# Kernel tuning notes

Hardware: AMD Instinct MI355X
Metric: run time of the kernel (lower is better)

## Reference

```python
import jax, jax.numpy as jnp
import numpy as np
import math

B, N, D, H, E, EDGE_DIM, GEO_DIM = 32, 256, 512, 8, 1024, 256, 64
HD = D // H

def _lin(x, W, b):
    return x @ W.T + b

def _ln(x, g, b):
    m = x.mean(-1, keepdims=True)
    v = ((x - m) ** 2).mean(-1, keepdims=True)
    return (x - m) * jax.lax.rsqrt(v + 1e-5) * g + b

def setup_inputs() -> dict:
    key = jax.random.key(0)
    ks = jax.random.split(key, 20)
    p = lambda k, s: jax.random.normal(k, s, jnp.float32) * 0.02
    inp = {
        'x': jax.random.normal(ks[0], (B, N, D), jnp.float32),
        'node_masks': jnp.ones((B, N), jnp.float32),
        'relation_edges': jax.random.randint(ks[1], (B, E, 2), 0, N),
        'relation_masks': (jax.random.uniform(ks[2], (B, E)) > 0.2).astype(jnp.float32),
        'relation_embeddings': jax.random.normal(ks[3], (B, E, EDGE_DIM), jnp.float32),
        'relation_geo_features': jax.random.normal(ks[4], (B, E, GEO_DIM), jnp.float32),
        'Wq': p(ks[5], (D, D)), 'bq': jnp.zeros((D,), jnp.float32),
        'Wk': p(ks[6], (D, D)), 'bk': jnp.zeros((D,), jnp.float32),
        'Wv': p(ks[7], (D, D)), 'bv': jnp.zeros((D,), jnp.float32),
        'W_eb': p(ks[8], (H, EDGE_DIM)), 'b_eb': jnp.zeros((H,), jnp.float32),
        'geo_ln_g': jnp.ones((GEO_DIM,), jnp.float32), 'geo_ln_b': jnp.zeros((GEO_DIM,), jnp.float32),
        'W_geo': p(ks[9], (H, GEO_DIM)), 'b_geo': jnp.zeros((H,), jnp.float32),
        'W_out': p(ks[10], (D, D)), 'b_out': jnp.zeros((D,), jnp.float32),
        'norm_g': jnp.ones((D,), jnp.float32), 'norm_b': jnp.zeros((D,), jnp.float32),
        'ff_ln_g': jnp.ones((D,), jnp.float32), 'ff_ln_b': jnp.zeros((D,), jnp.float32),
        'W_ff1': p(ks[11], (4 * D, D)), 'b_ff1': jnp.zeros((4 * D,), jnp.float32),
        'W_ff2': p(ks[12], (D, 4 * D)), 'b_ff2': jnp.zeros((D,), jnp.float32),
    }
    return inp

def reference(x, node_masks, relation_edges, relation_masks, relation_embeddings,
              relation_geo_features, Wq, bq, Wk, bk, Wv, bv, W_eb, b_eb,
              geo_ln_g, geo_ln_b, W_geo, b_geo, W_out, b_out, norm_g, norm_b,
              ff_ln_g, ff_ln_b, W_ff1, b_ff1, W_ff2, b_ff2):
    residual = x
    xn = _ln(x, norm_g, norm_b)
    q = _lin(xn, Wq, bq).reshape(B, N, H, HD)
    k = _lin(xn, Wk, bk).reshape(B, N, H, HD)
    v = _lin(xn, Wv, bv).reshape(B, N, H, HD)
    attn = jnp.einsum('bihd,bjhd->bhij', q, k) / math.sqrt(HD)

    nm = node_masks.astype(bool)
    pair_mask = nm[:, None, :, None] & nm[:, None, None, :]  # [B,1,N,N]

    valid = relation_masks.astype(bool)  # [B,E]
    idx = jnp.clip(relation_edges.astype(jnp.int32), 0, N - 1)
    src, dst = idx[..., 0], idx[..., 1]
    # route invalid edges to padding index N (sliced away after scatter)
    src_w = jnp.where(valid, src, N)
    dst_w = jnp.where(valid, dst, N)
    b_idx = jnp.broadcast_to(jnp.arange(B)[:, None], (B, E))

    adj = jnp.zeros((B, N + 1, N + 1), bool).at[:, :N, :N].set(jnp.eye(N, dtype=bool))
    adj = adj.at[b_idx, src_w, dst_w].set(True).at[b_idx, dst_w, src_w].set(True)
    rel_adj = adj[:, None, :N, :N]  # [B,1,N,N]

    eb = _lin(relation_embeddings, W_eb, b_eb)  # [B,E,H]
    gb = _lin(_ln(relation_geo_features, geo_ln_g, geo_ln_b), W_geo, b_geo)
    total_bias = (eb + gb).transpose(0, 2, 1)  # [B,H,E]
    bb = jnp.broadcast_to(b_idx[:, None, :], (B, H, E))
    hh = jnp.broadcast_to(jnp.arange(H)[None, :, None], (B, H, E))
    ss = jnp.broadcast_to(src_w[:, None, :], (B, H, E))
    dd = jnp.broadcast_to(dst_w[:, None, :], (B, H, E))
    rb = jnp.zeros((B, H, N + 1, N + 1), x.dtype)
    rb = rb.at[bb, hh, ss, dd].set(total_bias).at[bb, hh, dd, ss].set(total_bias)
    attn = attn + rb[:, :, :N, :N]

    mask = pair_mask & rel_adj
    attn = jnp.where(mask, attn, jnp.finfo(attn.dtype).min)
    attn = jnp.nan_to_num(jax.nn.softmax(attn, axis=-1))
    out = jnp.einsum('bhij,bjhd->bihd', attn, v).reshape(B, N, D)
    x2 = residual + _lin(out, W_out, b_out)
    h1 = jax.nn.silu(_lin(_ln(x2, ff_ln_g, ff_ln_b), W_ff1, b_ff1))
    x3 = x2 + _lin(h1, W_ff2, b_ff2)
    return x3 * node_masks[..., None]
```

## Files before the change

### kernel.cpp

```cpp
#include <hip/hip_runtime.h>

#define B_ 32
#define N_ 256
#define D_ 512
#define H_ 8
#define E_ 1024
#define HD_ 64

using u16 = unsigned short;
typedef short bf8_t __attribute__((ext_vector_type(8)));
typedef float f4_t __attribute__((ext_vector_type(4)));

__device__ __forceinline__ u16 f2bf(float f) {
  union { float f; unsigned u; } x; x.f = f;
  unsigned r = x.u + 0x7fffu + ((x.u >> 16) & 1u);
  return (u16)(r >> 16);
}
__device__ __forceinline__ float bf2f(u16 x) {
  union { unsigned u; float f; } y; y.u = ((unsigned)x) << 16; return y.f;
}
__device__ __forceinline__ f4_t mfma16(bf8_t a, bf8_t b, f4_t c) {
  return __builtin_amdgcn_mfma_f32_16x16x32_bf16(a, b, c, 0, 0, 0);
}
__device__ __forceinline__ void gload_lds16(const u16* g, u16* s) {
  __builtin_amdgcn_global_load_lds((const __attribute__((address_space(1))) void*)g,
                                   (__attribute__((address_space(3))) void*)s, 16, 0, 0);
}

__global__ __launch_bounds__(256) void prep_kernel(
    const float* __restrict__ wq, const float* __restrict__ wk,
    const float* __restrict__ wv, const float* __restrict__ wo,
    const float* __restrict__ w1, const float* __restrict__ w2,
    u16* __restrict__ dq, u16* __restrict__ dk, u16* __restrict__ dv,
    u16* __restrict__ dox, u16* __restrict__ d1, u16* __restrict__ d2,
    const float* __restrict__ x, const float* __restrict__ ng,
    const float* __restrict__ nb, u16* __restrict__ xn,
    const int* __restrict__ edges, const float* __restrict__ rmask,
    int* __restrict__ win,
    const float* __restrict__ remb, const float* __restrict__ rgeo,
    const float* __restrict__ Web, const float* __restrict__ beb,
    const float* __restrict__ glng, const float* __restrict__ glnb,
    const float* __restrict__ Wgeo, const float* __restrict__ bgeo,
    float* __restrict__ tb) {
  __shared__ float red[8];
  __shared__ u16 sWeb[16 * 256];
  __shared__ u16 sWgeo[16 * 64];
  __shared__ float sLgb[128];
  const int t = threadIdx.x;
  const int blk0 = blockIdx.x;

  if (blk0 < 3072) {
    int blk = blk0;
    const float* src; u16* dst;
    if (blk < 256)        { src = wq; dst = dq; }
    else if (blk < 512)   { src = wk; dst = dk; blk -= 256; }
    else if (blk < 768)   { src = wv; dst = dv; blk -= 512; }
    else if (blk < 1024)  { src = wo; dst = dox; blk -= 768; }
    else if (blk < 2048)  { src = w1; dst = d1; blk -= 1024; }
    else                  { src = w2; dst = d2; blk -= 2048; }
    const int i = (blk * 256 + t) * 4;
    const float4 v = *(const float4*)(src + i);
    ushort4 o;
    o.x = f2bf(v.x); o.y = f2bf(v.y); o.z = f2bf(v.z); o.w = f2bf(v.w);
    *(ushort4*)(dst + i) = o;
  } else if (blk0 < 11264) {
    const int row = blk0 - 3072;
    const float* xr = x + (size_t)row * D_;
    float v0 = xr[t], v1 = xr[t + 256];
    float s = v0 + v1, ss = v0 * v0 + v1 * v1;
    #pragma unroll
    for (int m = 1; m < 64; m <<= 1) { s += __shfl_xor(s, m, 64); ss += __shfl_xor(ss, m, 64); }
    const int wave = t >> 6, lane = t & 63;
    if (!lane) { red[wave] = s; red[wave + 4] = ss; }
    __syncthreads();
    s = red[0] + red[1] + red[2] + red[3];
    ss = red[4] + red[5] + red[6] + red[7];
    const float mean = s * (1.f / D_);
    const float var = ss * (1.f / D_) - mean * mean;
    const float rs = rsqrtf(var + 1e-5f);
    xn[(size_t)row * D_ + t] = f2bf((v0 - mean) * rs * ng[t] + nb[t]);
    xn[(size_t)row * D_ + t + 256] = f2bf((v1 - mean) * rs * ng[t + 256] + nb[t + 256]);
  } else if (blk0 < 11392) {
    const int idx = (blk0 - 11264) * 256 + t;
    if (rmask[idx] != 0.f) {
      const int b = idx >> 10, e = idx & (E_ - 1);
      int s = edges[2 * idx], d = edges[2 * idx + 1];
      s = min(max(s, 0), N_ - 1);
      d = min(max(d, 0), N_ - 1);
      int* wb = win + (size_t)b * N_ * N_;
      atomicMax(&wb[s * N_ + d], e);
      atomicMax(&wb[d * N_ + s], E_ + e);
    }
  } else {
    const int eblk = blk0 - 11392;
    for (int i = t; i < 2048; i += 256) { sWeb[i] = f2bf(Web[i]); sWeb[2048 + i] = 0; }
    for (int i = t; i < 512; i += 256)  { sWgeo[i] = f2bf(Wgeo[i]); sWgeo[512 + i] = 0; }
    if (t < 64) { sLgb[t] = glng[t]; sLgb[64 + t] = glnb[t]; }
    __syncthreads();
    const int wave = t >> 6, lane = t & 63;
    const int am = lane & 15, quad = lane >> 4;
    const int e0 = eblk * 64 + wave * 16;

    f4_t acc = f4_t{0.f, 0.f, 0.f, 0.f};
    const float* ar = remb + (size_t)(e0 + am) * 256 + quad * 8;
    #pragma unroll
    for (int kt = 0; kt < 256; kt += 32) {
      const float4 p0 = *(const float4*)(ar + kt);
      const float4 p1 = *(const float4*)(ar + kt + 4);
      bf8_t a;
      a[0] = (short)f2bf(p0.x); a[1] = (short)f2bf(p0.y);
      a[2] = (short)f2bf(p0.z); a[3] = (short)f2bf(p0.w);
      a[4] = (short)f2bf(p1.x); a[5] = (short)f2bf(p1.y);
      a[6] = (short)f2bf(p1.z); a[7] = (short)f2bf(p1.w);
      const bf8_t bv = *(const bf8_t*)&sWeb[am * 256 + kt + quad * 8];
      acc = mfma16(a, bv, acc);
    }
    const float* gr = rgeo + (size_t)(e0 + am) * 64;
    float v[16];
    {
      const float4 p0 = *(const float4*)(gr + quad * 8);
      const float4 p1 = *(const float4*)(gr + quad * 8 + 4);
      const float4 p2 = *(const float4*)(gr + 32 + quad * 8);
      const float4 p3 = *(const float4*)(gr + 32 + quad * 8 + 4);
      v[0] = p0.x; v[1] = p0.y; v[2] = p0.z; v[3] = p0.w;
      v[4] = p1.x; v[5] = p1.y; v[6] = p1.z; v[7] = p1.w;
      v[8] = p2.x; v[9] = p2.y; v[10] = p2.z; v[11] = p2.w;
      v[12] = p3.x; v[13] = p3.y; v[14] = p3.z; v[15] = p3.w;
    }
    float s = 0.f, ss = 0.f;
    #pragma unroll
    for (int j = 0; j < 16; ++j) { s += v[j]; ss += v[j] * v[j]; }
    s += __shfl_xor(s, 16, 64);  ss += __shfl_xor(ss, 16, 64);
    s += __shfl_xor(s, 32, 64);  ss += __shfl_xor(ss, 32, 64);
    const float mean = s * (1.f / 64.f);
    const float rs = rsqrtf(ss * (1.f / 64.f) - mean * mean + 1e-5f);
    bf8_t a2, a3;
    #pragma unroll
    for (int j = 0; j < 8; ++j) {
      a2[j] = (short)f2bf((v[j] - mean) * rs * sLgb[quad * 8 + j] + sLgb[64 + quad * 8 + j]);
      a3[j] = (short)f2bf((v[8 + j] - mean) * rs * sLgb[32 + quad * 8 + j] +
                          sLgb[96 + quad * 8 + j]);
    }
    acc = mfma16(a2, *(const bf8_t*)&sWgeo[am * 64 + quad * 8], acc);
    acc = mfma16(a3, *(const bf8_t*)&sWgeo[am * 64 + 32 + quad * 8], acc);
    if (am < 8) {
      const float bias_v = beb[am] + bgeo[am];
      #pragma unroll
      for (int r = 0; r < 4; ++r) {
        const int eg = e0 + quad * 4 + r;
        tb[(size_t)((eg >> 10) * H_ + am) * E_ + (eg & (E_ - 1))] = acc[r] + bias_v;
      }
    }
  }
}

__global__ __launch_bounds__(256) void ln_kernel(const float* __restrict__ x,
                                                 const float* __restrict__ g,
                                                 const float* __restrict__ bta,
                                                 u16* __restrict__ out) {
  const int row = blockIdx.x, t = threadIdx.x;
  const float* xr = x + (size_t)row * D_;
  float v0 = xr[t], v1 = xr[t + 256];
  float s = v0 + v1, ss = v0 * v0 + v1 * v1;
  #pragma unroll
  for (int m = 1; m < 64; m <<= 1) { s += __shfl_xor(s, m, 64); ss += __shfl_xor(ss, m, 64); }
  __shared__ float red[8];
  const int wave = t >> 6, lane = t & 63;
  if (!lane) { red[wave] = s; red[wave + 4] = ss; }
  __syncthreads();
  s = red[0] + red[1] + red[2] + red[3];
  ss = red[4] + red[5] + red[6] + red[7];
  const float mean = s * (1.f / D_);
  const float var = ss * (1.f / D_) - mean * mean;
  const float rs = rsqrtf(var + 1e-5f);
  out[(size_t)row * D_ + t] = f2bf((v0 - mean) * rs * g[t] + bta[t]);
  out[(size_t)row * D_ + t + 256] = f2bf((v1 - mean) * rs * g[t + 256] + bta[t + 256]);
}

__global__ __launch_bounds__(256) void attn_kernel(
    const u16* __restrict__ q, const u16* __restrict__ k, const u16* __restrict__ v,
    const float* __restrict__ tb, const int* __restrict__ win,
    const float* __restrict__ nm, u16* __restrict__ out) {
  const int t = threadIdx.x;
  const int wave = t >> 6, lane = t & 63;
  const int g = blockIdx.x * 4 + wave;
  const int b = g >> 8, row = g & (N_ - 1);
  u16* op = out + (size_t)g * D_ + lane * 8;
  const float nmr = nm[g];
  if (nmr == 0.f) {
    bf8_t z = 0;
    *(bf8_t*)op = z;
    return;
  }
  float qf[8];
  {
    const bf8_t qv = *(const bf8_t*)(q + (size_t)g * D_ + lane * 8);
    #pragma unroll
    for (int j = 0; j < 8; ++j) qf[j] = bf2f((u16)qv[j]);
  }
  int4 w4 = *(const int4*)(win + (size_t)g * N_ + lane * 4);
  if (lane == (row >> 2)) {
    const int sl = row & 3;
    if (sl == 0)      { if (w4.x == -1) w4.x = 0x7FFFFFFF; }
    else if (sl == 1) { if (w4.y == -1) w4.y = 0x7FFFFFFF; }
    else if (sl == 2) { if (w4.z == -1) w4.z = 0x7FFFFFFF; }
    else              { if (w4.w == -1) w4.w = 0x7FFFFFFF; }
  }
  const float* tbh = tb + (size_t)(b * H_ + (lane >> 3)) * E_;
  const float* nmb = nm + b * N_;
  const u16* kb = k + (size_t)b * N_ * D_;
  const u16* vb = v + (size_t)b * N_ * D_;
  float m = -3.402823466e38f, sum = 0.f;
  float o[8];
  #pragma unroll
  for (int j = 0; j < 8; ++j) o[j] = 0.f;
  #pragma unroll
  for (int c = 0; c < 4; ++c) {
    const int wc = (c == 0) ? w4.x : (c == 1) ? w4.y : (c == 2) ? w4.z : w4.w;
    unsigned long long mk = __ballot(wc != -1);
    while (mk) {
      const int jl = __builtin_ctzll(mk);
      mk &= mk - 1;
      const int col = jl * 4 + c;
      const int wv = __shfl(wc, jl, 64);
      const float nmc = nmb[col];
      if (nmc == 0.f) continue;
      const bf8_t kv = *(const bf8_t*)(kb + (size_t)col * D_ + lane * 8);
      float d = 0.f;
      #pragma unroll
      for (int j = 0; j < 8; ++j) d += qf[j] * bf2f((u16)kv[j]);
      d += __shfl_xor(d, 1, 64);
      d += __shfl_xor(d, 2, 64);
      d += __shfl_xor(d, 4, 64);
      float s = d * 0.125f;
      if ((unsigned)wv < 2048u) s += tbh[wv & (E_ - 1)];
      const bf8_t vv = *(const bf8_t*)(vb + (size_t)col * D_ + lane * 8);
      if (s > m) {
        const float sc = __expf(m - s);
        sum *= sc;
        #pragma unroll
        for (int j = 0; j < 8; ++j) o[j] *= sc;
        m = s;
      }
      const float p = __expf(s - m);
      sum += p;
      #pragma unroll
      for (int j = 0; j < 8; ++j) o[j] += p * bf2f((u16)vv[j]);
    }
  }
  const float rinv = 1.f / sum;
  bf8_t res;
  #pragma unroll
  for (int j = 0; j < 8; ++j) res[j] = (short)f2bf(o[j] * rinv);
  *(bf8_t*)op = res;
}

template <int MODE, int BN>
__global__ __launch_bounds__(256, 2) void gemm_k(
    const u16* __restrict__ A,
    const u16* __restrict__ W0, const u16* __restrict__ W1, const u16* __restrict__ W2,
    const float* __restrict__ b0, const float* __restrict__ b1, const float* __restrict__ b2,
    void* d0, void* d1, void* d2,
    const void* res, const float* __restrict__ nmask, int K) {
  constexpr int MJ = BN / 32;
  constexpr int CB = BN / 32;
  __shared__ u16 As[128 * 64];
  __shared__ u16 Bs[BN * 64];
  const int tid = threadIdx.x;
  const int wave = tid >> 6, lane = tid & 63;
  const int am = lane & 15, quad = lane >> 4;
  const int m0 = blockIdx.x * 128;
  int n0, proj = 0;
  const u16* W;
  const float* bias;
  if constexpr (MODE == 0) {
    proj = blockIdx.y >> 2;
    n0 = (blockIdx.y & 3) * BN;
    W = proj == 0 ? W0 : (proj == 1 ? W1 : W2);
    bias = proj == 0 ? b0 : (proj == 1 ? b1 : b2);
  } else {
    n0 = blockIdx.y * BN;
    W = W0;
    bias = b0;
  }
  const int wm = (wave >> 1) * 64;
  const int wn = (wave & 1) * (BN / 2);

  f4_t acc[4][MJ];
  #pragma unroll
  for (int i = 0; i < 4; ++i)
    #pragma unroll
    for (int j = 0; j < MJ; ++j) acc[i][j] = f4_t{0.f, 0.f, 0.f, 0.f};

  int arow[4], aq[4], brow[CB], bq[CB];
  #pragma unroll
  for (int c = 0; c < 4; ++c) {
    const int g = (wave * 4 + c) * 64 + lane;
    arow[c] = g >> 3;
    aq[c] = (g & 7) ^ (arow[c] & 7);
  }
  #pragma unroll
  for (int c = 0; c < CB; ++c) {
    const int g = (wave * CB + c) * 64 + lane;
    brow[c] = g >> 3;
    bq[c] = (g & 7) ^ (brow[c] & 7);
  }

  for (int kt = 0; kt < K; kt += 64) {
    #pragma unroll
    for (int c = 0; c < 4; ++c)
      gload_lds16(A + (size_t)(m0 + arow[c]) * K + kt + aq[c] * 8, &As[(wave * 4 + c) * 512]);
    #pragma unroll
    for (int c = 0; c < CB; ++c)
      gload_lds16(W + (size_t)(n0 + brow[c]) * K + kt + bq[c] * 8, &Bs[(wave * CB + c) * 512]);
    __syncthreads();
    #pragma unroll
    for (int kc = 0; kc < 2; ++kc) {
      bf8_t af[4], bfv[MJ];
      #pragma unroll
      for (int i = 0; i < 4; ++i) {
        const int r = wm + i * 16 + am;
        af[i] = *(const bf8_t*)&As[r * 64 + (((kc * 4 + quad) ^ (r & 7)) * 8)];
      }
      #pragma unroll
      for (int j = 0; j < MJ; ++j) {
        const int r = wn + j * 16 + am;
        bfv[j] = *(const bf8_t*)&Bs[r * 64 + (((kc * 4 + quad) ^ (r & 7)) * 8)];
      }
      #pragma unroll
      for (int i = 0; i < 4; ++i)
        #pragma unroll
        for (int j = 0; j < MJ; ++j) acc[i][j] = mfma16(af[i], bfv[j], acc[i][j]);
    }
    __syncthreads();
  }

  const int cb = n0 + wn + am;
  const int rb = m0 + wm + quad * 4;
  #pragma unroll
  for (int j = 0; j < MJ; ++j) {
    const int col = cb + j * 16;
    const float bv = bias[col];
    #pragma unroll
    for (int i = 0; i < 4; ++i) {
      #pragma unroll
      for (int r = 0; r < 4; ++r) {
        const int row = rb + i * 16 + r;
        float v = acc[i][j][r] + bv;
        if constexpr (MODE == 0) {
          u16* dst = (u16*)(proj == 0 ? d0 : (proj == 1 ? d1 : d2));
          dst[(size_t)row * D_ + col] = f2bf(v);
        } else if constexpr (MODE == 2) {
          v += ((const float*)res)[(size_t)row * D_ + col];
          ((float*)d0)[(size_t)row * D_ + col] = v;
        } else if constexpr (MODE == 3) {
          v = v / (1.f + __expf(-v));
          ((u16*)d0)[(size_t)row * 2048 + col] = f2bf(v);
        } else {
          v += ((const float*)res)[(size_t)row * D_ + col];
          v *= nmask[row];
          ((float*)d0)[(size_t)row * D_ + col] = v;
        }
      }
    }
  }
}

extern "C" void kernel_launch(void* const* d_in, const int* in_sizes, int n_in,
                              void* d_out, int out_size, void* d_ws, size_t ws_size,
                              hipStream_t stream) {
  const float* x     = (const float*)d_in[0];
  const float* nm    = (const float*)d_in[1];
  const int*   edges = (const int*)d_in[2];
  const float* rmask = (const float*)d_in[3];
  const float* remb  = (const float*)d_in[4];
  const float* rgeo  = (const float*)d_in[5];
  const float* Wq = (const float*)d_in[6];  const float* bq = (const float*)d_in[7];
  const float* Wk = (const float*)d_in[8];  const float* bk = (const float*)d_in[9];
  const float* Wv = (const float*)d_in[10]; const float* bv = (const float*)d_in[11];
  const float* Web = (const float*)d_in[12]; const float* beb = (const float*)d_in[13];
  const float* glng = (const float*)d_in[14]; const float* glnb = (const float*)d_in[15];
  const float* Wgeo = (const float*)d_in[16]; const float* bgeo = (const float*)d_in[17];
  const float* Wout = (const float*)d_in[18]; const float* bout = (const float*)d_in[19];
  const float* ng = (const float*)d_in[20]; const float* nb = (const float*)d_in[21];
  const float* fg = (const float*)d_in[22]; const float* fb = (const float*)d_in[23];
  const float* Wff1 = (const float*)d_in[24]; const float* bff1 = (const float*)d_in[25];
  const float* Wff2 = (const float*)d_in[26]; const float* bff2 = (const float*)d_in[27];

  char* ws = (char*)d_ws;
  u16*   xn      = (u16*)(ws + 0);
  u16*   qb      = (u16*)(ws + 8388608);
  u16*   kb      = (u16*)(ws + 16777216);
  u16*   vb      = (u16*)(ws + 25165824);
  u16*   h1      = (u16*)(ws + 0);
  int*   win     = (int*)(ws + 33554432);
  u16*   x2n     = (u16*)(ws + 33554432);
  float* tb      = (float*)(ws + 41943040);
  u16* Wq16   = (u16*)(ws + 42991616);
  u16* Wk16   = (u16*)(ws + 43515904);
  u16* Wv16   = (u16*)(ws + 44040192);
  u16* Wout16 = (u16*)(ws + 44564480);
  u16* Wff116 = (u16*)(ws + 45088768);
  u16* Wff216 = (u16*)(ws + 47185920);
  u16*   attnout = xn;
  float* out     = (float*)d_out;

  hipMemsetAsync(win, 0xFF, (size_t)B_ * N_ * N_ * sizeof(int), stream);
  prep_kernel<<<11904, 256, 0, stream>>>(
      Wq, Wk, Wv, Wout, Wff1, Wff2, Wq16, Wk16, Wv16, Wout16, Wff116, Wff216,
      x, ng, nb, xn,
      edges, rmask, win,
      remb, rgeo, Web, beb, glng, glnb, Wgeo, bgeo, tb);
  gemm_k<0, 128><<<dim3(64, 12), 256, 0, stream>>>(xn, Wq16, Wk16, Wv16, bq, bk, bv,
                                                   (void*)qb, (void*)kb, (void*)vb,
                                                   nullptr, nullptr, D_);
  attn_kernel<<<dim3(B_ * N_ / 4), 256, 0, stream>>>(qb, kb, vb, tb, win, nm, attnout);
  gemm_k<2, 64><<<dim3(64, 8), 256, 0, stream>>>(attnout, Wout16, nullptr, nullptr,
                                                 bout, nullptr, nullptr,
                                                 (void*)out, nullptr, nullptr,
                                                 (const void*)x, nullptr, D_);
  ln_kernel<<<B_ * N_, 256, 0, stream>>>(out, fg, fb, x2n);
  gemm_k<3, 128><<<dim3(64, 16), 256, 0, stream>>>(x2n, Wff116, nullptr, nullptr,
                                                   bff1, nullptr, nullptr,
                                                   (void*)h1, nullptr, nullptr, nullptr, nullptr, D_);
  gemm_k<4, 64><<<dim3(64, 8), 256, 0, stream>>>(h1, Wff216, nullptr, nullptr,
                                                 bff2, nullptr, nullptr,
                                                 (void*)out, nullptr, nullptr,
                                                 (const void*)out, nm, 2048);
}
```

Baseline: 301.7 us.

## Double-buffer LDS tiles in GEMM kernel to overlap loads with MFMA

Splits the shared-memory A and B tiles into two buffers and issues the global-to-LDS loads for the next K tile before computing on the current one, with a single barrier per iteration. This is meant to hide global-load latency behind MFMA work. The MODE 0 projection index is also generalised to use 512/BN. In exchange, LDS use per block doubles, which may lower occupancy under launch_bounds(256,2).

```diff
diff --git a/kernel.cpp b/kernel.cpp
--- a/kernel.cpp
+++ b/kernel.cpp
@@ -264,8 +264,8 @@
     const void* res, const float* __restrict__ nmask, int K) {
   constexpr int MJ = BN / 32;
   constexpr int CB = BN / 32;
-  __shared__ u16 As[128 * 64];
-  __shared__ u16 Bs[BN * 64];
+  __shared__ u16 As[2][128 * 64];
+  __shared__ u16 Bs[2][BN * 64];
   const int tid = threadIdx.x;
   const int wave = tid >> 6, lane = tid & 63;
   const int am = lane & 15, quad = lane >> 4;
@@ -274,8 +274,9 @@
   const u16* W;
   const float* bias;
   if constexpr (MODE == 0) {
-    proj = blockIdx.y >> 2;
-    n0 = (blockIdx.y & 3) * BN;
+    constexpr int NPB = 512 / BN;
+    proj = blockIdx.y / NPB;
+    n0 = (blockIdx.y % NPB) * BN;
     W = proj == 0 ? W0 : (proj == 1 ? W1 : W2);
     bias = proj == 0 ? b0 : (proj == 1 ? b1 : b2);
   } else {
@@ -306,26 +307,39 @@
     bq[c] = (g & 7) ^ (brow[c] & 7);
   }
 
+  #pragma unroll
+  for (int c = 0; c < 4; ++c)
+    gload_lds16(A + (size_t)(m0 + arow[c]) * K + aq[c] * 8, &As[0][(wave * 4 + c) * 512]);
+  #pragma unroll
+  for (int c = 0; c < CB; ++c)
+    gload_lds16(W + (size_t)(n0 + brow[c]) * K + bq[c] * 8, &Bs[0][(wave * CB + c) * 512]);
+  __syncthreads();
+
+  int cur = 0;
   for (int kt = 0; kt < K; kt += 64) {
-    #pragma unroll
-    for (int c = 0; c < 4; ++c)
-      gload_lds16(A + (size_t)(m0 + arow[c]) * K + kt + aq[c] * 8, &As[(wave * 4 + c) * 512]);
-    #pragma unroll
-    for (int c = 0; c < CB; ++c)
-      gload_lds16(W + (size_t)(n0 + brow[c]) * K + kt + bq[c] * 8, &Bs[(wave * CB + c) * 512]);
-    __syncthreads();
+    const int nxt = cur ^ 1;
+    if (kt + 64 < K) {
+      #pragma unroll
+      for (int c = 0; c < 4; ++c)
+        gload_lds16(A + (size_t)(m0 + arow[c]) * K + (kt + 64) + aq[c] * 8,
+                    &As[nxt][(wave * 4 + c) * 512]);
+      #pragma unroll
+      for (int c = 0; c < CB; ++c)
+        gload_lds16(W + (size_t)(n0 + brow[c]) * K + (kt + 64) + bq[c] * 8,
+                    &Bs[nxt][(wave * CB + c) * 512]);
+    }
     #pragma unroll
     for (int kc = 0; kc < 2; ++kc) {
       bf8_t af[4], bfv[MJ];
       #pragma unroll
       for (int i = 0; i < 4; ++i) {
         const int r = wm + i * 16 + am;
-        af[i] = *(const bf8_t*)&As[r * 64 + (((kc * 4 + quad) ^ (r & 7)) * 8)];
+        af[i] = *(const bf8_t*)&As[cur][r * 64 + (((kc * 4 + quad) ^ (r & 7)) * 8)];
       }
       #pragma unroll
       for (int j = 0; j < MJ; ++j) {
         const int r = wn + j * 16 + am;
-        bfv[j] = *(const bf8_t*)&Bs[r * 64 + (((kc * 4 + quad) ^ (r & 7)) * 8)];
+        bfv[j] = *(const bf8_t*)&Bs[cur][r * 64 + (((kc * 4 + quad) ^ (r & 7)) * 8)];
       }
       #pragma unroll
       for (int i = 0; i < 4; ++i)
@@ -333,6 +347,7 @@
         for (int j = 0; j < MJ; ++j) acc[i][j] = mfma16(af[i], bfv[j], acc[i][j]);
     }
     __syncthreads();
+    cur = nxt;
   }
 
   const int cb = n0 + wn + am;
```

After: 309.0 us. 1.02x slower.
